# Kernel tuning notes

Measured on AMD Instinct MI355X. Metric: run time of the kernel, lower is better.

## Reference

```python
import jax, jax.numpy as jnp
import numpy as np

M = 128      # grid length
J = 80       # number of functional features (hard-coded *80 in module)
NB = 2       # n_base (module-level global used in forward)
N = NB * J   # total tiny basis networks = 160
H = 256      # hidden width
B = 2048     # batch
LN_EPS = 1e-6


def _layernorm(z, alpha, beta):
    # torch LayerNorm variant: std is UNBIASED (torch.std default), eps added to std
    avg = z.mean(axis=-1, keepdims=True)
    std = jnp.sqrt(z.var(axis=-1, ddof=1, keepdims=True)) + LN_EPS
    return (z - avg) / std * alpha + beta


def setup_inputs() -> dict:
    key = jax.random.key(0)
    ks = jax.random.split(key, 10)
    bh = 1.0 / np.sqrt(H)  # torch Linear default init bound for fan_in=H
    u = lambda k, shp, b: jax.random.uniform(k, shp, jnp.float32, -b, b)
    return {
        "x": jax.random.normal(ks[0], (B, M, J), jnp.float32),
        "t": jnp.linspace(0.0, 1.0, M, dtype=jnp.float32),
        "W_in": u(ks[1], (N, 1, H), 1.0),        # fan_in = 1
        "b_in": u(ks[2], (N, H), 1.0),
        "W_h": u(ks[3], (3, N, H, H), bh),        # 3 hidden->hidden linears
        "b_h": u(ks[4], (3, N, H), bh),
        "W_out": u(ks[5], (N, H, 1), bh),
        "b_out": u(ks[6], (N, 1), bh),
        "ln_alpha": jax.random.normal(ks[7], (4, N, H), jnp.float32),
        "ln_beta": jax.random.normal(ks[8], (4, N, H), jnp.float32),
    }


def reference(x, t, W_in, b_in, W_h, b_h, W_out, b_out, ln_alpha, ln_beta):
    # --- evaluate all N tiny basis MLPs on the grid, batched ---
    # input layer: t (M,) x W_in (N,1,H) -> (N, M, H)
    z = jnp.einsum("m,nh->nmh", t, W_in[:, 0, :]) + b_in[:, None, :]
    z = z + _layernorm(z, ln_alpha[0][:, None, :], ln_beta[0][:, None, :])
    z = jax.nn.selu(z)  # dropout is identity in eval mode
    for i in range(3):
        z = jnp.einsum("nmh,nhk->nmk", z, W_h[i]) + b_h[i][:, None, :]
        z = z + _layernorm(z, ln_alpha[i + 1][:, None, :], ln_beta[i + 1][:, None, :])
        z = jax.nn.selu(z)
    bases = jnp.einsum("nmh,nh->nm", z, W_out[:, :, 0]) + b_out  # (N, M)

    # --- trapezoidal inner-product score ---
    h = t[1:] - t[:-1]                                   # (M-1,)
    w = jnp.zeros(M, x.dtype).at[:-1].add(h / 2).at[1:].add(h / 2)  # trapezoid weights
    bases_r = bases.reshape(J, NB, M)                    # basis i*NB+k serves feature i
    score = jnp.einsum("bmj,jkm,m->bjk", x, bases_r, w)  # (B, J, NB)
    return score.reshape(x.shape[0], J * NB)
```

## Files before the change

### kernel.cpp

```cpp
#include <hip/hip_runtime.h>
#include <math.h>

#define M_GRID 128
#define J_FEAT 80
#define NNET   160
#define HDIM   256

typedef __attribute__((ext_vector_type(8))) short v8s;
typedef __attribute__((ext_vector_type(4))) float f4;

__device__ __forceinline__ unsigned short f2bf(float f) {
    unsigned u = __float_as_uint(f);
    u += 0x7fffu + ((u >> 16) & 1u);
    return (unsigned short)(u >> 16);
}

__device__ __forceinline__ float selu_f(float x) {
    const float SC = 1.0507009873554805f;
    const float AL = 1.6732632423543772f;
    return x > 0.f ? SC * x : SC * AL * (__expf(x) - 1.f);
}

__attribute__((amdgpu_flat_work_group_size(512, 512)))
__global__ void basis_kernel(const float* __restrict__ t,
                             const float* __restrict__ W_in,
                             const float* __restrict__ b_in,
                             const float* __restrict__ W_h,
                             const float* __restrict__ b_h,
                             const float* __restrict__ W_out,
                             const float* __restrict__ b_out,
                             const float* __restrict__ ln_a,
                             const float* __restrict__ ln_b,
                             float* __restrict__ basesT)
{
    extern __shared__ __align__(16) unsigned char lds[];
    const int n    = blockIdx.x;
    const int tid  = threadIdx.x;
    const int l    = tid & 63;
    const int wv   = tid >> 6;
    const int lr   = l & 15;
    const int g    = l >> 4;
    const int jcol = tid & 255;
    const int o8   = tid >> 8;

    unsigned char* const actw = lds + 81920 + (size_t)wv * 8192;
    float* const P = (float*)(lds + 147456);

    {
        const size_t nb = (size_t)n * HDIM;
        #pragma unroll
        for (int i = 0; i < 7; ++i) {
            const int idx = tid + (i << 9), grp = idx >> 8, off = idx & 255;
            float v;
            if (grp == 0)       v = W_out[nb + off];
            else if (grp < 4)   v = ln_a[((size_t)grp * NNET + n) * HDIM + off];
            else if (grp < 7)   v = ln_b[((size_t)(grp - 3) * NNET + n) * HDIM + off];
            else if (grp < 10)  v = b_h[((size_t)(grp - 7) * NNET + n) * HDIM + off];
            else if (grp == 10) v = W_in[nb + off];
            else if (grp == 11) v = b_in[nb + off];
            else if (grp == 12) v = ln_a[nb + off];
            else                v = ln_b[nb + off];
            P[idx] = v;
        }
    }
    __syncthreads();

    auto issue = [&](int q) {
        unsigned char* dst = lds + ((size_t)(q & 1) << 15);
        const float* Wq = W_h + ((size_t)((q >> 3) * NNET + n) << 16)
                        + (size_t)(q & 7) * 32 * HDIM + (l << 2);
        #pragma unroll
        for (int i = 0; i < 4; ++i) {
            const int r = wv * 4 + i;
            __builtin_amdgcn_global_load_lds(
                (const __attribute__((address_space(1))) void*)(Wq + (size_t)r * HDIM),
                (__attribute__((address_space(3))) void*)(dst + (size_t)r * 1024),
                16, 0, 0);
        }
    };
    auto convert = [&](int q) {
        const unsigned char* src = lds + ((size_t)(q & 1) << 15);
        #pragma unroll
        for (int o = 0; o < 2; ++o) {
            v8s pk;
            #pragma unroll
            for (int i2 = 0; i2 < 8; ++i2) {
                const int k = o8 * 16 + o * 8 + i2;
                pk[i2] = (short)f2bf(*(const float*)(src + (size_t)k * 1024 + (jcol << 2)));
            }
            int byte = 65536 + (o8 << 13) + jcol * 32 + (o << 4);
            byte ^= ((jcol >> 2) & 7) << 4;
            *(v8s*)(lds + byte) = pk;
        }
    };

    issue(0);
    issue(1);

    const float tval = t[wv * 16 + lr];
    {
        const float* wi = P + 2560; const float* bi = P + 2816;
        const float* la = P + 3072; const float* lb = P + 3328;
        float s_ = 0.f, q_ = 0.f;
        #pragma unroll
        for (int kt = 0; kt < 8; ++kt) {
            const int h0 = kt * 32 + g * 8;
            const f4 w0 = *(const f4*)(wi + h0), w1 = *(const f4*)(wi + h0 + 4);
            const f4 b0 = *(const f4*)(bi + h0), b1 = *(const f4*)(bi + h0 + 4);
            #pragma unroll
            for (int i = 0; i < 4; ++i) {
                float v0 = __builtin_fmaf(tval, w0[i], b0[i]);
                float v1 = __builtin_fmaf(tval, w1[i], b1[i]);
                s_ += v0 + v1; q_ += v0 * v0 + v1 * v1;
            }
        }
        s_ += __shfl_xor(s_, 16); q_ += __shfl_xor(q_, 16);
        s_ += __shfl_xor(s_, 32); q_ += __shfl_xor(q_, 32);
        const float mean = s_ * (1.f / 256.f);
        const float var  = (q_ - s_ * s_ * (1.f / 256.f)) * (1.f / 255.f);
        const float inv  = 1.f / (sqrtf(var) + 1e-6f);
        asm volatile("" ::: "memory");
        #pragma unroll
        for (int kt = 0; kt < 8; ++kt) {
            const int h0 = kt * 32 + g * 8;
            const f4 w0 = *(const f4*)(wi + h0), w1 = *(const f4*)(wi + h0 + 4);
            const f4 b0 = *(const f4*)(bi + h0), b1 = *(const f4*)(bi + h0 + 4);
            const f4 a0 = *(const f4*)(la + h0), a1 = *(const f4*)(la + h0 + 4);
            const f4 e0 = *(const f4*)(lb + h0), e1 = *(const f4*)(lb + h0 + 4);
            v8s a;
            #pragma unroll
            for (int i = 0; i < 4; ++i) {
                float v0 = __builtin_fmaf(tval, w0[i], b0[i]);
                float v1 = __builtin_fmaf(tval, w1[i], b1[i]);
                a[i]     = (short)f2bf(selu_f(v0 + (v0 - mean) * inv * a0[i] + e0[i]));
                a[i + 4] = (short)f2bf(selu_f(v1 + (v1 - mean) * inv * a1[i] + e1[i]));
            }
            *(v8s*)(actw + ((lr * 512 + h0 * 2) ^ (lr << 5))) = a;
        }
        asm volatile("s_waitcnt lgkmcnt(0)" ::: "memory");
        __builtin_amdgcn_sched_barrier(0);
    }

    f4 acc[16];

    #pragma unroll 1
    for (int L = 0; L < 3; ++L) {
        const f4 zero = {0.f, 0.f, 0.f, 0.f};
        #pragma unroll
        for (int ct = 0; ct < 16; ++ct) acc[ct] = zero;

        #pragma unroll
        for (int s = 0; s < 8; ++s) {
            if (L == 2 && s == 7) asm volatile("s_waitcnt vmcnt(0)" ::: "memory");
            else                  asm volatile("s_waitcnt vmcnt(4)" ::: "memory");
            __builtin_amdgcn_sched_barrier(0);
            __builtin_amdgcn_s_barrier();
            __builtin_amdgcn_sched_barrier(0);
            convert(L * 8 + s);
            asm volatile("s_waitcnt lgkmcnt(0)" ::: "memory");
            __builtin_amdgcn_sched_barrier(0);
            __builtin_amdgcn_s_barrier();
            __builtin_amdgcn_sched_barrier(0);
            if (L * 8 + s + 2 < 24) issue(L * 8 + s + 2);
            const v8s af = *(const v8s*)(actw + ((lr * 512 + (s * 32 + g * 8) * 2) ^ (lr << 5)));
            #pragma unroll
            for (int ct = 0; ct < 16; ++ct) {
                const int jb = ct * 16 + lr;
                int byte = 65536 + ((g >> 1) << 13) + jb * 32 + ((g & 1) << 4);
                byte ^= ((jb >> 2) & 7) << 4;
                const v8s bf = *(const v8s*)(lds + byte);
                acc[ct] = __builtin_amdgcn_mfma_f32_16x16x32_bf16(af, bf, acc[ct], 0, 0, 0);
            }
        }

        const float* bh = P + (7 + L) * 256;
        const float* la = P + (1 + L) * 256;
        const float* lb = P + (4 + L) * 256;

        float sums[4] = {0,0,0,0}, sqs[4] = {0,0,0,0};
        #pragma unroll
        for (int ct = 0; ct < 16; ++ct) {
            const float bias = bh[ct * 16 + lr];
            #pragma unroll
            for (int r = 0; r < 4; ++r) {
                float v = acc[ct][r] + bias;
                acc[ct][r] = v;
                sums[r] += v; sqs[r] += v * v;
            }
        }
        #pragma unroll
        for (int r = 0; r < 4; ++r)
            #pragma unroll
            for (int m = 1; m <= 8; m <<= 1) {
                sums[r] += __shfl_xor(sums[r], m);
                sqs[r]  += __shfl_xor(sqs[r],  m);
            }
        float mean[4], inv[4];
        #pragma unroll
        for (int r = 0; r < 4; ++r) {
            mean[r] = sums[r] * (1.f / 256.f);
            float var = (sqs[r] - sums[r] * sums[r] * (1.f / 256.f)) * (1.f / 255.f);
            inv[r] = 1.f / (sqrtf(var) + 1e-6f);
        }

        if (L < 2) {
            #pragma unroll
            for (int ct = 0; ct < 16; ++ct) {
                const float a_ = la[ct * 16 + lr], b_ = lb[ct * 16 + lr];
                #pragma unroll
                for (int r = 0; r < 4; ++r) {
                    float v  = acc[ct][r];
                    float sv = selu_f(v + (v - mean[r]) * inv[r] * a_ + b_);
                    const int row = 4 * g + r;
                    *(unsigned short*)(actw + ((row * 512 + (ct * 16 + lr) * 2) ^ (row << 5)))
                        = f2bf(sv);
                }
            }
            asm volatile("s_waitcnt lgkmcnt(0)" ::: "memory");
            __builtin_amdgcn_sched_barrier(0);
        } else {
            const float bo = b_out[n];
            float ps[4] = {0,0,0,0};
            #pragma unroll
            for (int ct = 0; ct < 16; ++ct) {
                const float a_ = la[ct * 16 + lr], b_ = lb[ct * 16 + lr];
                const float w_ = P[ct * 16 + lr];
                #pragma unroll
                for (int r = 0; r < 4; ++r) {
                    float v  = acc[ct][r];
                    float sv = selu_f(v + (v - mean[r]) * inv[r] * a_ + b_);
                    ps[r] += sv * w_;
                }
            }
            #pragma unroll
            for (int r = 0; r < 4; ++r)
                #pragma unroll
                for (int m = 1; m <= 8; m <<= 1)
                    ps[r] += __shfl_xor(ps[r], m);
            #pragma unroll
            for (int r = 0; r < 4; ++r)
                if (lr == r)
                    basesT[(size_t)(wv * 16 + 4 * g + r) * NNET + n] = ps[r] + bo;
        }
    }
}

__launch_bounds__(256)
__global__ void score_kernel(const float* __restrict__ x,
                             const float* __restrict__ t,
                             const float* __restrict__ basesT,
                             float* __restrict__ out)
{
    __shared__ float c_lds[M_GRID * 32];
    const int jt  = blockIdx.x;
    const int bt  = blockIdx.y;
    const int tid = threadIdx.x;

    for (int i = tid; i < M_GRID * 32; i += 256) {
        const int m  = i >> 5;
        const int jl = i & 31;
        const float tp = t[m == M_GRID - 1 ? M_GRID - 1 : m + 1];
        const float tm = t[m == 0 ? 0 : m - 1];
        c_lds[i] = basesT[(size_t)m * NNET + jt * 32 + jl] * 0.5f * (tp - tm);
    }
    __syncthreads();

    const int jj = tid & 31;
    const int bs = tid >> 5;
    const int jk = jt * 32 + jj;
    const int b  = bt * 8 + bs;
    const float* xp = x + (size_t)b * (M_GRID * J_FEAT) + (jk >> 1);
    float acc = 0.f;
    #pragma unroll 8
    for (int m = 0; m < M_GRID; ++m)
        acc += xp[(size_t)m * J_FEAT] * c_lds[m * 32 + jj];
    out[(size_t)b * NNET + jk] = acc;
}

extern "C" void kernel_launch(void* const* d_in, const int* in_sizes, int n_in,
                              void* d_out, int out_size, void* d_ws, size_t ws_size,
                              hipStream_t stream)
{
    const float* x     = (const float*)d_in[0];
    const float* t     = (const float*)d_in[1];
    const float* W_in  = (const float*)d_in[2];
    const float* b_in  = (const float*)d_in[3];
    const float* W_h   = (const float*)d_in[4];
    const float* b_h   = (const float*)d_in[5];
    const float* W_out = (const float*)d_in[6];
    const float* b_out = (const float*)d_in[7];
    const float* ln_a  = (const float*)d_in[8];
    const float* ln_b  = (const float*)d_in[9];
    float* basesT = (float*)d_ws;

    basis_kernel<<<dim3(NNET), dim3(512), 161792, stream>>>(
        t, W_in, b_in, W_h, b_h, W_out, b_out, ln_a, ln_b, basesT);
    score_kernel<<<dim3(5, 256), dim3(256), 0, stream>>>(
        x, t, basesT, (float*)d_out);
}
```

Before: 77.81 us.

## Prefetch W_h tiles into registers with triple buffering instead of global_load_lds

Measured after the change: 112.3 us. 1.44x slower.

```diff
diff --git a/kernel.cpp b/kernel.cpp
--- a/kernel.cpp
+++ b/kernel.cpp
@@ -43,8 +43,8 @@
     const int jcol = tid & 255;
     const int o8   = tid >> 8;
 
-    unsigned char* const actw = lds + 81920 + (size_t)wv * 8192;
-    float* const P = (float*)(lds + 147456);
+    unsigned char* const actw = lds + 32768 + (size_t)wv * 8192;
+    float* const P = (float*)(lds + 98304);
 
     {
         const size_t nb = (size_t)n * HDIM;
@@ -65,37 +65,29 @@
     }
     __syncthreads();
 
-    auto issue = [&](int q) {
-        unsigned char* dst = lds + ((size_t)(q & 1) << 15);
+    float rr[3][16];
+    auto issue = [&](float (&r)[16], int q) {
         const float* Wq = W_h + ((size_t)((q >> 3) * NNET + n) << 16)
-                        + (size_t)(q & 7) * 32 * HDIM + (l << 2);
-        #pragma unroll
-        for (int i = 0; i < 4; ++i) {
-            const int r = wv * 4 + i;
-            __builtin_amdgcn_global_load_lds(
-                (const __attribute__((address_space(1))) void*)(Wq + (size_t)r * HDIM),
-                (__attribute__((address_space(3))) void*)(dst + (size_t)r * 1024),
-                16, 0, 0);
-        }
+                        + (size_t)((q & 7) * 32 + o8 * 16) * HDIM + jcol;
+        #pragma unroll
+        for (int i = 0; i < 16; ++i) r[i] = Wq[(size_t)i * HDIM];
     };
-    auto convert = [&](int q) {
-        const unsigned char* src = lds + ((size_t)(q & 1) << 15);
+    auto write_tile = [&](float (&r)[16], int buf) {
         #pragma unroll
         for (int o = 0; o < 2; ++o) {
             v8s pk;
             #pragma unroll
-            for (int i2 = 0; i2 < 8; ++i2) {
-                const int k = o8 * 16 + o * 8 + i2;
-                pk[i2] = (short)f2bf(*(const float*)(src + (size_t)k * 1024 + (jcol << 2)));
-            }
-            int byte = 65536 + (o8 << 13) + jcol * 32 + (o << 4);
+            for (int i = 0; i < 8; ++i) pk[i] = (short)f2bf(r[o * 8 + i]);
+            int byte = (buf << 14) + (o8 << 13) + jcol * 32 + (o << 4);
             byte ^= ((jcol >> 2) & 7) << 4;
             *(v8s*)(lds + byte) = pk;
         }
     };
 
-    issue(0);
-    issue(1);
+    issue(rr[0], 0);
+    issue(rr[1], 1);
+    issue(rr[2], 2);
+    __builtin_amdgcn_sched_barrier(0);
 
     const float tval = t[wv * 16 + lr];
     {
@@ -137,40 +129,44 @@
             }
             *(v8s*)(actw + ((lr * 512 + h0 * 2) ^ (lr << 5))) = a;
         }
-        asm volatile("s_waitcnt lgkmcnt(0)" ::: "memory");
-        __builtin_amdgcn_sched_barrier(0);
-    }
+    }
+
+    write_tile(rr[0], 0);
+    issue(rr[0], 3);
+    asm volatile("s_waitcnt lgkmcnt(0)" ::: "memory");
+    __builtin_amdgcn_sched_barrier(0);
+    __builtin_amdgcn_s_barrier();
 
     f4 acc[16];
 
-    #pragma unroll 1
+    #pragma unroll
     for (int L = 0; L < 3; ++L) {
         const f4 zero = {0.f, 0.f, 0.f, 0.f};
         #pragma unroll
-        for (int ct = 0; ct < 16; ++ct) acc[ct] = zero;
-
-        #pragma unroll
-        for (int s = 0; s < 8; ++s) {
-            if (L == 2 && s == 7) asm volatile("s_waitcnt vmcnt(0)" ::: "memory");
-            else                  asm volatile("s_waitcnt vmcnt(4)" ::: "memory");
-            __builtin_amdgcn_sched_barrier(0);
-            __builtin_amdgcn_s_barrier();
-            __builtin_amdgcn_sched_barrier(0);
-            convert(L * 8 + s);
+        for (int ct = 0; ct < 16; ++ct) {
+            acc[ct] = zero;
+            asm volatile("" : "+a"(acc[ct]));
+        }
+
+        #pragma unroll
+        for (int s8 = 0; s8 < 8; ++s8) {
+            const int s = L * 8 + s8;
+            if (s < 23) {
+                write_tile(rr[(s + 1) % 3], (s + 1) & 1);
+                if (s + 4 < 24) issue(rr[(s + 1) % 3], s + 4);
+            }
+            const v8s af = *(const v8s*)(actw + ((lr * 512 + (s8 * 32 + g * 8) * 2) ^ (lr << 5)));
+            #pragma unroll
+            for (int ct = 0; ct < 16; ++ct) {
+                const int jb = ct * 16 + lr;
+                int byte = ((s & 1) << 14) + ((g >> 1) << 13) + jb * 32 + ((g & 1) << 4);
+                byte ^= ((jb >> 2) & 7) << 4;
+                const v8s bf = *(const v8s*)(lds + byte);
+                acc[ct] = __builtin_amdgcn_mfma_f32_16x16x32_bf16(af, bf, acc[ct], 0, 0, 0);
+            }
             asm volatile("s_waitcnt lgkmcnt(0)" ::: "memory");
             __builtin_amdgcn_sched_barrier(0);
             __builtin_amdgcn_s_barrier();
-            __builtin_amdgcn_sched_barrier(0);
-            if (L * 8 + s + 2 < 24) issue(L * 8 + s + 2);
-            const v8s af = *(const v8s*)(actw + ((lr * 512 + (s * 32 + g * 8) * 2) ^ (lr << 5)));
-            #pragma unroll
-            for (int ct = 0; ct < 16; ++ct) {
-                const int jb = ct * 16 + lr;
-                int byte = 65536 + ((g >> 1) << 13) + jb * 32 + ((g & 1) << 4);
-                byte ^= ((jb >> 2) & 7) << 4;
-                const v8s bf = *(const v8s*)(lds + byte);
-                acc[ct] = __builtin_amdgcn_mfma_f32_16x16x32_bf16(af, bf, acc[ct], 0, 0, 0);
-            }
         }
 
         const float* bh = P + (7 + L) * 256;
@@ -293,7 +289,7 @@
     const float* ln_b  = (const float*)d_in[9];
     float* basesT = (float*)d_ws;
 
-    basis_kernel<<<dim3(NNET), dim3(512), 161792, stream>>>(
+    basis_kernel<<<dim3(NNET), dim3(512), 112640, stream>>>(
         t, W_in, b_in, W_h, b_h, W_out, b_out, ln_a, ln_b, basesT);
     score_kernel<<<dim3(5, 256), dim3(256), 0, stream>>>(
         x, t, basesT, (float*)d_out);
```
